# Kernel tuning notes

Measured on AMD Instinct MI355X. Metric: run time of the kernel, lower is better.

Reference implementation:

```python
import jax, jax.numpy as jnp
import numpy as np

NUM_CLASSES = 20
C = 64          # channels
K = 48          # patch_size
H = 4           # num_heads
D = C // H      # head dim = 16
N = 192000      # total points (multiple of K -> padding is identity)
P = N // K      # number of patches = 4000
POS_BND = 11    # int((4*48)**(1/3)*2)
RPE_NUM = 2 * POS_BND + 1  # 23
SCALE = D ** (-0.5)
LN_EPS = 1e-5


def setup_inputs() -> dict:
    key = jax.random.key(0)
    ks = jax.random.split(key, 24)
    w = lambda k, shape: (jax.random.normal(k, shape, jnp.float32) * 0.02)
    inp = {}
    inp["seg_logits"] = jax.random.normal(ks[0], (N, NUM_CLASSES), jnp.float32)
    inp["coord"] = jax.random.uniform(ks[1], (N, 3), jnp.float32)
    order = jax.random.permutation(ks[2], N).astype(jnp.int32)
    inp["serialized_order"] = order
    inp["serialized_inverse"] = jnp.argsort(order).astype(jnp.int32)
    inp["grid_coord"] = jax.random.randint(ks[3], (N, 3), 0, 64, jnp.int32)
    # learned parameters
    inp["W_in"] = w(ks[4], (NUM_CLASSES + 3, C)); inp["b_in"] = jnp.zeros((C,), jnp.float32)
    inp["g1"] = jnp.ones((C,), jnp.float32); inp["be1"] = jnp.zeros((C,), jnp.float32)
    inp["W_qkv"] = w(ks[5], (C, 3 * C)); inp["b_qkv"] = jnp.zeros((3 * C,), jnp.float32)
    inp["rpe"] = w(ks[6], (3 * RPE_NUM, H))
    inp["W_attn"] = w(ks[7], (C, C)); inp["b_attn"] = jnp.zeros((C,), jnp.float32)
    inp["g2"] = jnp.ones((C,), jnp.float32); inp["be2"] = jnp.zeros((C,), jnp.float32)
    inp["W_f1"] = w(ks[8], (C, 4 * C)); inp["b_f1"] = jnp.zeros((4 * C,), jnp.float32)
    inp["W_f2"] = w(ks[9], (4 * C, C)); inp["b_f2"] = jnp.zeros((C,), jnp.float32)
    inp["W_h1"] = w(ks[10], (C, C // 2)); inp["b_h1"] = jnp.zeros((C // 2,), jnp.float32)
    inp["W_h2"] = w(ks[11], (C // 2, 3)); inp["b_h2"] = jnp.zeros((3,), jnp.float32)
    return inp


def _ln(x, g, b):
    m = x.mean(-1, keepdims=True)
    v = jnp.var(x, axis=-1, keepdims=True)
    return (x - m) * jax.lax.rsqrt(v + LN_EPS) * g + b


def reference(seg_logits, coord, serialized_order, serialized_inverse, grid_coord,
              W_in, b_in, g1, be1, W_qkv, b_qkv, rpe, W_attn, b_attn,
              g2, be2, W_f1, b_f1, W_f2, b_f2, W_h1, b_h1, W_h2, b_h2):
    # softmax(seg_logits) + coord -> input projection
    sem = jax.nn.softmax(seg_logits, axis=-1)
    feat = jnp.concatenate([sem, coord], axis=-1) @ W_in + b_in        # (N, C)

    # All per-batch counts are multiples of K, so pad/unpad are identity;
    # order/inverse are just the serialization permutation.
    qkv = (_ln(feat, g1, be1) @ W_qkv + b_qkv)[serialized_order]       # (N, 3C)
    qkv = qkv.reshape(P, K, 3, H, D)
    q = qkv[:, :, 0].transpose(0, 2, 1, 3)                             # (P, H, K, D)
    k = qkv[:, :, 1].transpose(0, 2, 1, 3)
    v = qkv[:, :, 2].transpose(0, 2, 1, 3)

    attn = jnp.einsum('phkd,phmd->phkm', q * SCALE, k)                 # (P, H, K, K)

    # relative position bias (computed under no_grad in the original)
    gc = grid_coord[serialized_order].reshape(P, K, 3)
    rel = gc[:, :, None, :] - gc[:, None, :, :]                        # (P, K, K, 3)
    idx = jnp.clip(rel, -POS_BND, POS_BND) + POS_BND + jnp.arange(3, dtype=rel.dtype) * RPE_NUM
    bias = rpe[idx[..., 0]] + rpe[idx[..., 1]] + rpe[idx[..., 2]]      # (P, K, K, H)
    attn = attn + jax.lax.stop_gradient(bias.transpose(0, 3, 1, 2))

    attn = jax.nn.softmax(attn.astype(jnp.float32), axis=-1).astype(qkv.dtype)
    out = jnp.einsum('phkm,phmd->pkhd', attn, v).reshape(N, C)

    attn_out = out[serialized_inverse] @ W_attn + b_attn
    feat = feat + attn_out
    h = _ln(feat, g2, be2)
    feat = feat + (jax.nn.gelu(h @ W_f1 + b_f1, approximate=False) @ W_f2 + b_f2)
    return jax.nn.gelu(feat @ W_h1 + b_h1, approximate=False) @ W_h2 + b_h2  # (N, 3)
```

## Files before the change

### kernel.cpp

```cpp
#include <hip/hip_runtime.h>
#include <hip/hip_fp16.h>
#include <math.h>

#define N_PTS   192000
#define NPATCH  4000
#define PK      48
#define NH      4
#define HD      16

__device__ __forceinline__ float erf_inl(float x) {
    float ax = fabsf(x);
    float t = 1.0f / fmaf(0.3275911f, ax, 1.0f);
    float poly = fmaf(1.061405429f, t, -1.453152027f);
    poly = fmaf(poly, t, 1.421413741f);
    poly = fmaf(poly, t, -0.284496736f);
    poly = fmaf(poly, t, 0.254829592f);
    poly *= t;
    float e = __expf(-ax * ax);
    float r = 1.0f - poly * e;
    return copysignf(r, x);
}

__device__ __forceinline__ float gelu_exact(float x) {
    return 0.5f * x * (1.0f + erf_inl(x * 0.70710678118654752f));
}

__global__ __launch_bounds__(256) void k_in_qkv(
    const float* __restrict__ seg, const float* __restrict__ coord,
    const float* __restrict__ W_in, const float* __restrict__ b_in,
    const float* __restrict__ g1, const float* __restrict__ be1,
    const float* __restrict__ W_qkv, const float* __restrict__ b_qkv,
    float* __restrict__ feat_out, float* __restrict__ qkv_out)
{
    int i = blockIdx.x * 256 + threadIdx.x;
    if (i >= N_PTS) return;

    float iv[23];
    {
        const float* s = seg + (size_t)i * 20;
        float mx = -1e30f;
        #pragma unroll
        for (int j = 0; j < 20; ++j) { iv[j] = s[j]; mx = fmaxf(mx, iv[j]); }
        float sum = 0.f;
        #pragma unroll
        for (int j = 0; j < 20; ++j) { iv[j] = __expf(iv[j] - mx); sum += iv[j]; }
        float r = 1.f / sum;
        #pragma unroll
        for (int j = 0; j < 20; ++j) iv[j] *= r;
        iv[20] = coord[(size_t)i*3 + 0];
        iv[21] = coord[(size_t)i*3 + 1];
        iv[22] = coord[(size_t)i*3 + 2];
    }

    float f[64];
    #pragma unroll
    for (int c = 0; c < 64; ++c) {
        float a = b_in[c];
        #pragma unroll
        for (int j = 0; j < 23; ++j) a = fmaf(iv[j], W_in[j*64 + c], a);
        f[c] = a;
    }
    {
        float4* fd = (float4*)(feat_out + (size_t)i * 64);
        #pragma unroll
        for (int c4 = 0; c4 < 16; ++c4)
            fd[c4] = make_float4(f[4*c4], f[4*c4+1], f[4*c4+2], f[4*c4+3]);
    }
    {
        float m = 0.f;
        #pragma unroll
        for (int c = 0; c < 64; ++c) m += f[c];
        m *= (1.f/64.f);
        float v = 0.f;
        #pragma unroll
        for (int c = 0; c < 64; ++c) { float d = f[c]-m; v = fmaf(d, d, v); }
        v *= (1.f/64.f);
        float rs = 1.f / sqrtf(v + 1e-5f);
        #pragma unroll
        for (int c = 0; c < 64; ++c) f[c] = (f[c]-m)*rs*g1[c] + be1[c];
    }
    {
        float* qd = qkv_out + (size_t)i * 192;
        for (int t4 = 0; t4 < 48; ++t4) {
            const float* bq = b_qkv + t4*4;
            float ax = bq[0], ay = bq[1], az = bq[2], aw = bq[3];
            const float* w = W_qkv + t4*4;
            #pragma unroll
            for (int c = 0; c < 64; ++c) {
                float h = f[c];
                const float* wr = w + c*192;
                ax = fmaf(h, wr[0], ax); ay = fmaf(h, wr[1], ay);
                az = fmaf(h, wr[2], az); aw = fmaf(h, wr[3], aw);
            }
            ((float4*)qd)[t4] = make_float4(ax, ay, az, aw);
        }
    }
}

__global__ __launch_bounds__(256) void k_attn(
    const float* __restrict__ qkv, const int* __restrict__ order,
    const int* __restrict__ grid_coord, const float* __restrict__ rpe,
    float* __restrict__ outb)
{
    __shared__ float q_s[NH][PK][17];
    __shared__ float k_s[NH][PK][HD];
    __shared__ float v_s[NH][PK][HD];
    __shared__ float rpe_s[276];
    __shared__ int   ord_s[PK];
    __shared__ int   gc_s[PK][3];

    int p = blockIdx.x;
    int tid = threadIdx.x;

    if (tid < PK) ord_s[tid] = order[p*PK + tid];
    for (int t = tid; t < 276; t += 256) {
        int hh2 = t / 69;
        int idx = t - hh2 * 69;
        rpe_s[t] = rpe[idx*4 + hh2];
    }
    __syncthreads();

    if (tid < PK) {
        int row = ord_s[tid];
        gc_s[tid][0] = grid_coord[(size_t)row*3 + 0];
        gc_s[tid][1] = grid_coord[(size_t)row*3 + 1];
        gc_s[tid][2] = grid_coord[(size_t)row*3 + 2];
    }
    {
        int lane = tid & 63;
        int hh = lane >> 4, dd = lane & 15;
        for (int rr = tid >> 6; rr < PK; rr += 4) {
            const float* src = qkv + (size_t)ord_s[rr] * 192;
            float qv = src[lane];
            float kv = src[64 + lane];
            float vv = src[128 + lane];
            q_s[hh][rr][dd] = qv;
            k_s[hh][rr][dd] = kv;
            v_s[hh][rr][dd] = vv;
        }
    }
    __syncthreads();

    int h = tid >> 6;
    int r = tid & 63;
    if (r >= PK) return;

    float qr[HD];
    #pragma unroll
    for (int d = 0; d < HD; ++d) qr[d] = q_s[h][r][d];
    int gx = gc_s[r][0], gy = gc_s[r][1], gz = gc_s[r][2];
    int h69 = h * 69;

    float m_run = -1e30f, l_run = 0.f;
    float acc[HD];
    #pragma unroll
    for (int d = 0; d < HD; ++d) acc[d] = 0.f;

    #pragma unroll 4
    for (int m = 0; m < PK; ++m) {
        float a = 0.f;
        #pragma unroll
        for (int d = 0; d < HD; ++d) a = fmaf(qr[d], k_s[h][m][d], a);
        a *= 0.25f;
        int i0 = min(max(gx - gc_s[m][0], -11), 11) + 11;
        int i1 = min(max(gy - gc_s[m][1], -11), 11) + 34;
        int i2 = min(max(gz - gc_s[m][2], -11), 11) + 57;
        a += rpe_s[h69 + i0] + rpe_s[h69 + i1] + rpe_s[h69 + i2];

        float m_new = fmaxf(m_run, a);
        float scale = __expf(m_run - m_new);
        float pvv   = __expf(a - m_new);
        l_run = fmaf(l_run, scale, pvv);
        #pragma unroll
        for (int d = 0; d < HD; ++d)
            acc[d] = fmaf(acc[d], scale, pvv * v_s[h][m][d]);
        m_run = m_new;
    }
    float rinv = 1.f / l_run;

    {
        float* dst = outb + (size_t)ord_s[r]*64 + h*HD;
        float4* d4 = (float4*)dst;
        #pragma unroll
        for (int d4i = 0; d4i < 4; ++d4i)
            d4[d4i] = make_float4(acc[4*d4i]*rinv, acc[4*d4i+1]*rinv,
                                  acc[4*d4i+2]*rinv, acc[4*d4i+3]*rinv);
    }
}

__global__ __launch_bounds__(256) void k_ffn(
    const float* __restrict__ outb, const float* __restrict__ featb,
    const float* __restrict__ W_attn, const float* __restrict__ b_attn,
    const float* __restrict__ g2, const float* __restrict__ be2,
    const float* __restrict__ W_f1, const float* __restrict__ b_f1,
    const float* __restrict__ W_f2, const float* __restrict__ b_f2,
    const float* __restrict__ W_h1, const float* __restrict__ b_h1,
    const float* __restrict__ W_h2, const float* __restrict__ b_h2,
    float* __restrict__ out)
{
    __shared__ __half shh[64][256];

    int tid = threadIdx.x;
    int i = blockIdx.x * 256 + tid;
    if (i >= N_PTS) return;

    float o[64];
    {
        const float4* os = (const float4*)(outb + (size_t)i * 64);
        #pragma unroll
        for (int c4 = 0; c4 < 16; ++c4) {
            float4 t = os[c4];
            o[4*c4]=t.x; o[4*c4+1]=t.y; o[4*c4+2]=t.z; o[4*c4+3]=t.w;
        }
    }
    float f[64];
    #pragma unroll
    for (int c = 0; c < 64; ++c) {
        float a = b_attn[c];
        #pragma unroll
        for (int k = 0; k < 64; ++k) a = fmaf(o[k], W_attn[k*64 + c], a);
        f[c] = a;
    }
    {
        const float4* fs = (const float4*)(featb + (size_t)i * 64);
        #pragma unroll
        for (int c4 = 0; c4 < 16; ++c4) {
            float4 t = fs[c4];
            f[4*c4]+=t.x; f[4*c4+1]+=t.y; f[4*c4+2]+=t.z; f[4*c4+3]+=t.w;
        }
    }
    {
        float m = 0.f;
        #pragma unroll
        for (int c = 0; c < 64; ++c) m += f[c];
        m *= (1.f/64.f);
        float v = 0.f;
        #pragma unroll
        for (int c = 0; c < 64; ++c) { float d = f[c]-m; v = fmaf(d, d, v); }
        v *= (1.f/64.f);
        float rs = 1.f / sqrtf(v + 1e-5f);
        #pragma unroll
        for (int c = 0; c < 64; ++c)
            shh[c][tid] = __float2half((f[c]-m)*rs*g2[c] + be2[c]);
    }
    #pragma unroll
    for (int c = 0; c < 64; ++c) f[c] += b_f2[c];
    for (int t0 = 0; t0 < 16; ++t0) {
        float a[16];
        #pragma unroll
        for (int tt = 0; tt < 16; ++tt) a[tt] = b_f1[t0*16 + tt];
        #pragma unroll
        for (int c = 0; c < 64; ++c) {
            float hv = __half2float(shh[c][tid]);
            const float* w = W_f1 + c*256 + t0*16;
            #pragma unroll
            for (int tt = 0; tt < 16; ++tt) a[tt] = fmaf(hv, w[tt], a[tt]);
        }
        #pragma unroll
        for (int tt = 0; tt < 16; ++tt) a[tt] = gelu_exact(a[tt]);
        #pragma unroll
        for (int tt = 0; tt < 16; ++tt) {
            float av = a[tt];
            const float* w2 = W_f2 + (t0*16 + tt)*64;
            #pragma unroll
            for (int c = 0; c < 64; ++c) f[c] = fmaf(av, w2[c], f[c]);
        }
    }
    float g[32];
    #pragma unroll
    for (int t = 0; t < 32; ++t) {
        float a = b_h1[t];
        #pragma unroll
        for (int c = 0; c < 64; ++c) a = fmaf(f[c], W_h1[c*32 + t], a);
        g[t] = gelu_exact(a);
    }
    #pragma unroll
    for (int r = 0; r < 3; ++r) {
        float a = b_h2[r];
        #pragma unroll
        for (int t = 0; t < 32; ++t) a = fmaf(g[t], W_h2[t*3 + r], a);
        out[(size_t)i*3 + r] = a;
    }
}

extern "C" void kernel_launch(void* const* d_in, const int* in_sizes, int n_in,
                              void* d_out, int out_size, void* d_ws, size_t ws_size,
                              hipStream_t stream)
{
    const float* seg    = (const float*)d_in[0];
    const float* coord  = (const float*)d_in[1];
    const int*   order  = (const int*)d_in[2];
    const int*   gc     = (const int*)d_in[4];
    const float* W_in   = (const float*)d_in[5];
    const float* b_in   = (const float*)d_in[6];
    const float* g1     = (const float*)d_in[7];
    const float* be1    = (const float*)d_in[8];
    const float* W_qkv  = (const float*)d_in[9];
    const float* b_qkv  = (const float*)d_in[10];
    const float* rpe    = (const float*)d_in[11];
    const float* W_attn = (const float*)d_in[12];
    const float* b_attn = (const float*)d_in[13];
    const float* g2     = (const float*)d_in[14];
    const float* be2    = (const float*)d_in[15];
    const float* W_f1   = (const float*)d_in[16];
    const float* b_f1   = (const float*)d_in[17];
    const float* W_f2   = (const float*)d_in[18];
    const float* b_f2   = (const float*)d_in[19];
    const float* W_h1   = (const float*)d_in[20];
    const float* b_h1   = (const float*)d_in[21];
    const float* W_h2   = (const float*)d_in[22];
    const float* b_h2   = (const float*)d_in[23];

    float* feat = (float*)d_ws;
    float* qkvb = feat + (size_t)N_PTS * 64;
    float* outw = qkvb + (size_t)N_PTS * 192;

    k_in_qkv<<<N_PTS/256, 256, 0, stream>>>(seg, coord, W_in, b_in, g1, be1,
                                            W_qkv, b_qkv, feat, qkvb);
    k_attn<<<NPATCH, 256, 0, stream>>>(qkvb, order, gc, rpe, outw);
    k_ffn<<<N_PTS/256, 256, 0, stream>>>(outw, feat, W_attn, b_attn, g2, be2,
                                         W_f1, b_f1, W_f2, b_f2,
                                         W_h1, b_h1, W_h2, b_h2, (float*)d_out);
}
```

Before: 657.0 us.

## Split FFN per point across two threads to cut register pressure

The FFN kernel now assigns two threads to each point. Each thread computes half the output channels of the attention projection and half of the hidden FFN units, then the halves are combined with shared-memory reductions for LayerNorm, the FFN output and the head projection. The grid doubles so that 128 points are handled per 256-thread block. The goal is to reduce per-thread register arrays so occupancy rises, at the cost of extra barriers, shared-memory exchanges and duplicated weight loads. LayerNorm variance now uses a single-pass E[x^2]-m^2 formula.

```diff
diff --git a/kernel.cpp b/kernel.cpp
--- a/kernel.cpp
+++ b/kernel.cpp
@@ -198,88 +198,146 @@
     const float* __restrict__ W_h2, const float* __restrict__ b_h2,
     float* __restrict__ out)
 {
-    __shared__ __half shh[64][256];
-
-    int tid = threadIdx.x;
-    int i = blockIdx.x * 256 + tid;
-    if (i >= N_PTS) return;
-
-    float o[64];
-    {
-        const float4* os = (const float4*)(outb + (size_t)i * 64);
-        #pragma unroll
-        for (int c4 = 0; c4 < 16; ++c4) {
-            float4 t = os[c4];
-            o[4*c4]=t.x; o[4*c4+1]=t.y; o[4*c4+2]=t.z; o[4*c4+3]=t.w;
-        }
-    }
-    float f[64];
-    #pragma unroll
-    for (int c = 0; c < 64; ++c) {
-        float a = b_attn[c];
-        #pragma unroll
-        for (int k = 0; k < 64; ++k) a = fmaf(o[k], W_attn[k*64 + c], a);
-        f[c] = a;
-    }
-    {
-        const float4* fs = (const float4*)(featb + (size_t)i * 64);
-        #pragma unroll
-        for (int c4 = 0; c4 < 16; ++c4) {
+    __shared__ __half shh[128][66];
+    __shared__ float  pex[2][16][128];
+    __shared__ float  sred[2][128][2];
+
+    int tid  = threadIdx.x;
+    int ptb  = tid & 127;
+    int half = tid >> 7;
+    int cb   = half * 32;
+    size_t i = (size_t)blockIdx.x * 128 + ptb;
+
+    float f[32];
+    #pragma unroll
+    for (int c = 0; c < 32; ++c) f[c] = b_attn[cb + c];
+    for (int kc = 0; kc < 4; ++kc) {
+        float o16[16];
+        const float4* os = (const float4*)(outb + i * 64 + kc * 16);
+        #pragma unroll
+        for (int q = 0; q < 4; ++q) {
+            float4 t = os[q];
+            o16[4*q]=t.x; o16[4*q+1]=t.y; o16[4*q+2]=t.z; o16[4*q+3]=t.w;
+        }
+        #pragma unroll
+        for (int j = 0; j < 16; ++j) {
+            float vv = o16[j];
+            const float* w = W_attn + (kc*16 + j)*64 + cb;
+            #pragma unroll
+            for (int c = 0; c < 32; ++c) f[c] = fmaf(vv, w[c], f[c]);
+        }
+    }
+    {
+        const float4* fs = (const float4*)(featb + i * 64 + cb);
+        #pragma unroll
+        for (int c4 = 0; c4 < 8; ++c4) {
             float4 t = fs[c4];
             f[4*c4]+=t.x; f[4*c4+1]+=t.y; f[4*c4+2]+=t.z; f[4*c4+3]+=t.w;
         }
     }
     {
-        float m = 0.f;
-        #pragma unroll
-        for (int c = 0; c < 64; ++c) m += f[c];
-        m *= (1.f/64.f);
-        float v = 0.f;
-        #pragma unroll
-        for (int c = 0; c < 64; ++c) { float d = f[c]-m; v = fmaf(d, d, v); }
-        v *= (1.f/64.f);
-        float rs = 1.f / sqrtf(v + 1e-5f);
-        #pragma unroll
-        for (int c = 0; c < 64; ++c)
-            shh[c][tid] = __float2half((f[c]-m)*rs*g2[c] + be2[c]);
-    }
-    #pragma unroll
-    for (int c = 0; c < 64; ++c) f[c] += b_f2[c];
-    for (int t0 = 0; t0 < 16; ++t0) {
+        float s0 = 0.f, q0 = 0.f;
+        #pragma unroll
+        for (int c = 0; c < 32; ++c) { s0 += f[c]; q0 = fmaf(f[c], f[c], q0); }
+        sred[half][ptb][0] = s0;
+        sred[half][ptb][1] = q0;
+    }
+    __syncthreads();
+    {
+        float S = sred[half^1][ptb][0] + sred[half][ptb][0];
+        float Q = sred[half^1][ptb][1] + sred[half][ptb][1];
+        float m = S * (1.f/64.f);
+        float var = Q * (1.f/64.f) - m * m;
+        float rs = 1.f / sqrtf(var + 1e-5f);
+        #pragma unroll
+        for (int c = 0; c < 32; ++c)
+            shh[ptb][cb + c] = __float2half((f[c]-m)*rs*g2[cb+c] + be2[cb+c]);
+    }
+    __syncthreads();
+
+    float p[64];
+    #pragma unroll
+    for (int c = 0; c < 64; ++c) p[c] = 0.f;
+    for (int ch = 0; ch < 8; ++ch) {
+        int hb = half * 128 + ch * 16;
         float a[16];
         #pragma unroll
-        for (int tt = 0; tt < 16; ++tt) a[tt] = b_f1[t0*16 + tt];
-        #pragma unroll
-        for (int c = 0; c < 64; ++c) {
-            float hv = __half2float(shh[c][tid]);
-            const float* w = W_f1 + c*256 + t0*16;
-            #pragma unroll
-            for (int tt = 0; tt < 16; ++tt) a[tt] = fmaf(hv, w[tt], a[tt]);
-        }
-        #pragma unroll
-        for (int tt = 0; tt < 16; ++tt) a[tt] = gelu_exact(a[tt]);
-        #pragma unroll
-        for (int tt = 0; tt < 16; ++tt) {
-            float av = a[tt];
-            const float* w2 = W_f2 + (t0*16 + tt)*64;
-            #pragma unroll
-            for (int c = 0; c < 64; ++c) f[c] = fmaf(av, w2[c], f[c]);
-        }
-    }
-    float g[32];
-    #pragma unroll
-    for (int t = 0; t < 32; ++t) {
-        float a = b_h1[t];
-        #pragma unroll
-        for (int c = 0; c < 64; ++c) a = fmaf(f[c], W_h1[c*32 + t], a);
-        g[t] = gelu_exact(a);
-    }
-    #pragma unroll
-    for (int r = 0; r < 3; ++r) {
-        float a = b_h2[r];
-        #pragma unroll
-        for (int t = 0; t < 32; ++t) a = fmaf(g[t], W_h2[t*3 + r], a);
-        out[(size_t)i*3 + r] = a;
+        for (int t = 0; t < 16; ++t) a[t] = b_f1[hb + t];
+        const __half2* hrow = (const __half2*)&shh[ptb][0];
+        #pragma unroll
+        for (int c2 = 0; c2 < 32; ++c2) {
+            __half2 hp = hrow[c2];
+            float h0 = __half2float(hp.x);
+            float h1 = __half2float(hp.y);
+            const float* w0 = W_f1 + (size_t)(2*c2) * 256 + hb;
+            #pragma unroll
+            for (int t = 0; t < 16; ++t) a[t] = fmaf(h0, w0[t], a[t]);
+            #pragma unroll
+            for (int t = 0; t < 16; ++t) a[t] = fmaf(h1, w0[256 + t], a[t]);
+        }
+        #pragma unroll
+        for (int t = 0; t < 16; ++t) a[t] = gelu_exact(a[t]);
+        #pragma unroll
+        for (int t = 0; t < 16; ++t) {
+            float av = a[t];
+            const float* w2 = W_f2 + (size_t)(hb + t) * 64;
+            #pragma unroll
+            for (int c = 0; c < 64; ++c) p[c] = fmaf(av, w2[c], p[c]);
+        }
+    }
+    int pcb = 32 - cb;
+    __syncthreads();
+    #pragma unroll
+    for (int j = 0; j < 16; ++j) pex[half][j][ptb] = p[pcb + j];
+    __syncthreads();
+    #pragma unroll
+    for (int j = 0; j < 16; ++j)
+        f[j] += b_f2[cb + j] + p[cb + j] + pex[half^1][j][ptb];
+    __syncthreads();
+    #pragma unroll
+    for (int j = 0; j < 16; ++j) pex[half][j][ptb] = p[pcb + 16 + j];
+    __syncthreads();
+    #pragma unroll
+    for (int j = 0; j < 16; ++j)
+        f[16+j] += b_f2[cb + 16 + j] + p[cb + 16 + j] + pex[half^1][j][ptb];
+
+    float gp[32];
+    #pragma unroll
+    for (int t = 0; t < 32; ++t) gp[t] = 0.f;
+    #pragma unroll
+    for (int c = 0; c < 32; ++c) {
+        float vv = f[c];
+        const float* w = W_h1 + (size_t)(cb + c) * 32;
+        #pragma unroll
+        for (int t = 0; t < 32; ++t) gp[t] = fmaf(vv, w[t], gp[t]);
+    }
+    __syncthreads();
+    if (half == 1) {
+        #pragma unroll
+        for (int j = 0; j < 16; ++j) pex[0][j][ptb] = gp[j];
+        #pragma unroll
+        for (int j = 0; j < 16; ++j) pex[1][j][ptb] = gp[16 + j];
+    }
+    __syncthreads();
+    if (half == 0) {
+        float g[32];
+        #pragma unroll
+        for (int t = 0; t < 16; ++t)
+            g[t] = gelu_exact(gp[t] + pex[0][t][ptb] + b_h1[t]);
+        #pragma unroll
+        for (int t = 0; t < 16; ++t)
+            g[16+t] = gelu_exact(gp[16+t] + pex[1][t][ptb] + b_h1[16+t]);
+        float r0 = b_h2[0], r1 = b_h2[1], r2 = b_h2[2];
+        #pragma unroll
+        for (int t = 0; t < 32; ++t) {
+            float gv = g[t];
+            r0 = fmaf(gv, W_h2[t*3 + 0], r0);
+            r1 = fmaf(gv, W_h2[t*3 + 1], r1);
+            r2 = fmaf(gv, W_h2[t*3 + 2], r2);
+        }
+        out[i*3 + 0] = r0;
+        out[i*3 + 1] = r1;
+        out[i*3 + 2] = r2;
     }
 }
 
@@ -318,7 +376,7 @@
     k_in_qkv<<<N_PTS/256, 256, 0, stream>>>(seg, coord, W_in, b_in, g1, be1,
                                             W_qkv, b_qkv, feat, qkvb);
     k_attn<<<NPATCH, 256, 0, stream>>>(qkvb, order, gc, rpe, outw);
-    k_ffn<<<N_PTS/256, 256, 0, stream>>>(outw, feat, W_attn, b_attn, g2, be2,
+    k_ffn<<<N_PTS/128, 256, 0, stream>>>(outw, feat, W_attn, b_attn, g2, be2,
                                          W_f1, b_f1, W_f2, b_f2,
                                          W_h1, b_h1, W_h2, b_h2, (float*)d_out);
 }
```

After: 1.448 ms. 2.2x slower.
